# Kernel optimization log

Hardware: AMD Instinct MI355X
Metric: run time of the kernel (lower is better)

Reference implementation:

```python
import jax, jax.numpy as jnp
import numpy as np

N_NODES = 100000
N_EDGES = 1600000
C_IN, C_HID, C_OUT = 128, 64, 32


def setup_inputs() -> dict:
    key = jax.random.key(0)
    kx, ke, kw1, kw2 = jax.random.split(key, 4)
    x = jax.random.normal(kx, (N_NODES, C_IN), dtype=jnp.float32)
    edge_index = jax.random.randint(ke, (2, N_EDGES), 0, N_NODES, dtype=jnp.int64)
    # Glorot-ish init for the two GCNConv linear weights; PyG GCNConv bias inits to zero.
    W1 = jax.random.normal(kw1, (C_IN, C_HID), dtype=jnp.float32) / np.sqrt(C_IN)
    b1 = jnp.zeros((C_HID,), dtype=jnp.float32)
    W2 = jax.random.normal(kw2, (C_HID, C_OUT), dtype=jnp.float32) / np.sqrt(C_HID)
    b2 = jnp.zeros((C_OUT,), dtype=jnp.float32)
    return {"x": x, "edge_index": edge_index, "W1": W1, "b1": b1, "W2": W2, "b2": b2}


def _gcn_conv(x, W, b, src, dst, num_nodes):
    """PyG GCNConv: add self-loops, symmetric norm D^-1/2 A D^-1/2, linear, aggregate, bias."""
    xw = x @ W  # [N, out]
    # degree at destination, including the self-loop contribution of 1 per node
    deg = jnp.zeros((num_nodes,), xw.dtype).at[dst].add(1.0) + 1.0
    dinv = jax.lax.rsqrt(deg)  # deg >= 1 thanks to self-loops
    norm = dinv[src] * dinv[dst]  # [E]
    # scatter-add messages from source nodes into destination nodes
    out = jnp.zeros_like(xw).at[dst].add(norm[:, None] * xw[src])
    # self-loop term: norm_ii = dinv[i]^2
    out = out + (dinv * dinv)[:, None] * xw
    return out + b


def reference(x, edge_index, W1, b1, W2, b2):
    src, dst = edge_index[0], edge_index[1]
    h = _gcn_conv(x, W1, b1, src, dst, N_NODES)
    h = jax.nn.relu(h)
    # Dropout(0.1) is identity in eval mode (deterministic reference)
    out = _gcn_conv(h, W2, b2, src, dst, N_NODES)
    return out
```

## Files before the change

kernel.cpp:

```cpp
#include <hip/hip_runtime.h>
#include <hip/hip_bf16.h>


#define C_IN  128
#define C_HID 64
#define C_OUT 32
#define BK_SHIFT 10
#define BK_NODES (1 << BK_SHIFT)
#define BK_MAXB  128
#define EPB 2048

typedef unsigned short ushort_t;
typedef __attribute__((ext_vector_type(8))) short bf16x8;
typedef __attribute__((ext_vector_type(4))) float f32x4;

__device__ inline ushort_t f2bf(float f) {
    __hip_bfloat16 b = __float2bfloat16(f);
    return *reinterpret_cast<ushort_t*>(&b);
}
__device__ inline float bflo(unsigned int v) { return __uint_as_float(v << 16); }
__device__ inline float bfhi(unsigned int v) { return __uint_as_float(v & 0xffff0000u); }


__global__ __launch_bounds__(256) void bucket_edges(
        const int* __restrict__ src, const int* __restrict__ dst,
        int* __restrict__ bcur, unsigned int* __restrict__ bucketed,
        int cap, int E, int nb) {
    __shared__ unsigned int stage[EPB];
    __shared__ unsigned char bkt[EPB];
    __shared__ int cnt[BK_MAXB];
    __shared__ int lofs[BK_MAXB];
    __shared__ int base[BK_MAXB];
    int tid = threadIdx.x;
    for (int i = tid; i < nb; i += 256) cnt[i] = 0;
    __syncthreads();
    int e0 = blockIdx.x * EPB;
    int myb[8]; int myr[8]; unsigned int mys[8];
    #pragma unroll
    for (int i = 0; i < 8; ++i) {
        int e = e0 + i * 256 + tid;
        if (e < E) {
            int d = dst[e];
            int s = src[e];
            int b = d >> BK_SHIFT;
            myb[i] = b;
            mys[i] = (unsigned int)s | ((unsigned int)(d & (BK_NODES - 1)) << 17);
            myr[i] = atomicAdd(&cnt[b], 1);
        } else myb[i] = -1;
    }
    __syncthreads();
    if (tid < 64) {
        int b0 = 2 * tid, b1 = 2 * tid + 1;
        int c0 = (b0 < nb) ? cnt[b0] : 0;
        int c1 = (b1 < nb) ? cnt[b1] : 0;
        int p = c0 + c1;
        int s = p;
        #pragma unroll
        for (int off = 1; off < 64; off <<= 1) {
            int t = __shfl_up(s, off, 64);
            if (tid >= off) s += t;
        }
        if (b0 < nb) lofs[b0] = s - p;
        if (b1 < nb) lofs[b1] = s - c1;
    }
    __syncthreads();
    #pragma unroll
    for (int i = 0; i < 8; ++i) {
        if (myb[i] >= 0) {
            int p = lofs[myb[i]] + myr[i];
            stage[p] = mys[i];
            bkt[p] = (unsigned char)myb[i];
        }
    }
    for (int i = tid; i < nb; i += 256)
        base[i] = atomicAdd(&bcur[i], cnt[i]);
    __syncthreads();
    int total = min(EPB, E - e0);
    for (int p = tid; p < total; p += 256) {
        int b = bkt[p];
        int di = base[b] + (p - lofs[b]);
        if (di < cap)
            bucketed[(size_t)b * cap + di] = stage[p];
    }
}

__global__ void scan_eb(const int* __restrict__ bcur, int* __restrict__ ebase,
                        int* __restrict__ offsets, int cap, int nb, int n) {
    __shared__ int wsum[2];
    int tid = threadIdx.x;
    int lane = tid & 63, wid = tid >> 6;
    int v = (tid < nb) ? min(bcur[tid], cap) : 0;
    int s = v;
    #pragma unroll
    for (int off = 1; off < 64; off <<= 1) {
        int t = __shfl_up(s, off, 64);
        if (lane >= off) s += t;
    }
    if (lane == 63) wsum[wid] = s;
    __syncthreads();
    int incl = s + ((wid == 1) ? wsum[0] : 0);
    if (tid < nb) ebase[tid] = incl - v;
    if (tid == nb - 1) { ebase[nb] = incl; offsets[n] = incl; }
}

__global__ __launch_bounds__(1024) void fill_csr_fused(
        const unsigned int* __restrict__ bucketed, const int* __restrict__ ebase,
        int* __restrict__ offsets, float* __restrict__ dinv,
        int* __restrict__ csr_src, int cap, int n) {
    __shared__ int hist[BK_NODES];
    __shared__ int wsum[16];
    int tid = threadIdx.x, lane = tid & 63, wid = tid >> 6;
    int b = blockIdx.x;
    int node0 = b << BK_SHIFT;
    int nn = min(BK_NODES, n - node0);
    int eb = ebase[b];
    int cnt = ebase[b + 1] - eb;
    const unsigned int* bp = bucketed + (size_t)b * cap;
    hist[tid] = 0;
    __syncthreads();
    for (int e = tid; e < cnt; e += 1024)
        atomicAdd(&hist[bp[e] >> 17], 1);
    __syncthreads();
    int v = hist[tid];
    int s = v;
    #pragma unroll
    for (int off = 1; off < 64; off <<= 1) {
        int t = __shfl_up(s, off, 64);
        if (lane >= off) s += t;
    }
    if (lane == 63) wsum[wid] = s;
    __syncthreads();
    if (wid == 0 && lane < 16) {
        int ws = wsum[lane];
        #pragma unroll
        for (int off = 1; off < 16; off <<= 1) {
            int t = __shfl_up(ws, off, 64);
            if (lane >= off) ws += t;
        }
        wsum[lane] = ws;
    }
    __syncthreads();
    int wpre = (wid > 0) ? wsum[wid - 1] : 0;
    int excl = wpre + s - v;
    if (tid < nn) {
        offsets[node0 + tid] = eb + excl;
        dinv[node0 + tid] = rsqrtf((float)v + 1.0f);
    }
    __syncthreads();
    hist[tid] = eb + excl;
    __syncthreads();
    for (int e = tid; e < cnt; e += 1024) {
        unsigned int u = bp[e];
        int pos = atomicAdd(&hist[u >> 17], 1);
        csr_src[pos] = (int)(u & 0x1FFFFu);
    }
}

__global__ void count_deg(const int* __restrict__ dst, int* __restrict__ deg, int E) {
    int idx = blockIdx.x * blockDim.x + threadIdx.x;
    int stride = gridDim.x * blockDim.x;
    for (int e = idx; e < E; e += stride)
        atomicAdd(&deg[dst[e]], 1);
}

__global__ void fill_csr(const int* __restrict__ src, const int* __restrict__ dst,
                         int* __restrict__ cursor, int* __restrict__ csr_src, int E) {
    int idx = blockIdx.x * blockDim.x + threadIdx.x;
    int stride = gridDim.x * blockDim.x;
    for (int e = idx; e < E; e += stride) {
        int pos = atomicAdd(&cursor[dst[e]], 1);
        csr_src[pos] = src[e];
    }
}

__global__ void scan_blocks(const int* __restrict__ deg, int* __restrict__ offsets,
                            int* __restrict__ bsums, float* __restrict__ dinv, int n) {
    __shared__ int wsum[16];
    int tid = threadIdx.x, lane = tid & 63, wid = tid >> 6;
    int i = blockIdx.x * 1024 + tid;
    int v = (i < n) ? deg[i] : 0;
    if (i < n) dinv[i] = rsqrtf((float)v + 1.0f);
    int s = v;
    #pragma unroll
    for (int off = 1; off < 64; off <<= 1) {
        int t = __shfl_up(s, off, 64);
        if (lane >= off) s += t;
    }
    if (lane == 63) wsum[wid] = s;
    __syncthreads();
    if (wid == 0 && lane < 16) {
        int ws = wsum[lane];
        #pragma unroll
        for (int off = 1; off < 16; off <<= 1) {
            int t = __shfl_up(ws, off, 64);
            if (lane >= off) ws += t;
        }
        wsum[lane] = ws;
        if (lane == 15) bsums[blockIdx.x] = ws;
    }
    __syncthreads();
    int wpre = (wid > 0) ? wsum[wid - 1] : 0;
    if (i < n) offsets[i] = wpre + s - v;
}

__global__ void scan_bsums(int* __restrict__ bsums, int nb) {
    __shared__ int wsum[16];
    int tid = threadIdx.x, lane = tid & 63, wid = tid >> 6;
    int v = (tid < nb) ? bsums[tid] : 0;
    int s = v;
    #pragma unroll
    for (int off = 1; off < 64; off <<= 1) {
        int t = __shfl_up(s, off, 64);
        if (lane >= off) s += t;
    }
    if (lane == 63) wsum[wid] = s;
    __syncthreads();
    if (wid == 0 && lane < 16) {
        int ws = wsum[lane];
        #pragma unroll
        for (int off = 1; off < 16; off <<= 1) {
            int t = __shfl_up(ws, off, 64);
            if (lane >= off) ws += t;
        }
        wsum[lane] = ws;
    }
    __syncthreads();
    int wpre = (wid > 0) ? wsum[wid - 1] : 0;
    if (tid < nb) bsums[tid] = wpre + s - v;
}

__global__ void scan_add(int* __restrict__ offsets, const int* __restrict__ bsums,
                         int n, int E) {
    int i = blockIdx.x * 1024 + threadIdx.x;
    if (i < n) offsets[i] += bsums[blockIdx.x];
    if (i == 0) offsets[n] = E;
}

__global__ __launch_bounds__(256) void gemm1_mfma(
        const float* __restrict__ x, const float* __restrict__ W1,
        const float* __restrict__ dinv, ushort_t* __restrict__ xws_bf, int n) {
    __shared__ ushort_t Xs[64 * 136];
    __shared__ ushort_t Wl[16 * 64 * 8];
    int tid = threadIdx.x;
    {
        const float4* Wv = reinterpret_cast<const float4*>(W1);
        #pragma unroll
        for (int p = 0; p < 8; ++p) {
            int idx = p * 256 + tid;
            float4 w = Wv[idx];
            int k = idx >> 4;
            int c0 = (idx & 15) * 4;
            ushort_t* d = &Wl[(k >> 3) * 512 + c0 * 8 + (k & 7)];
            d[0]  = f2bf(w.x);
            d[8]  = f2bf(w.y);
            d[16] = f2bf(w.z);
            d[24] = f2bf(w.w);
        }
    }
    int row0 = blockIdx.x * 64;
    {
        const float4* xv = reinterpret_cast<const float4*>(x + (size_t)row0 * C_IN);
        int maxv = min(64, n - row0) * (C_IN / 4);
        #pragma unroll
        for (int p = 0; p < 8; ++p) {
            int idx = p * 256 + tid;
            float4 v = (idx < maxv) ? xv[idx] : float4{0.f, 0.f, 0.f, 0.f};
            int row = idx >> 5, k4 = idx & 31;
            ushort4 pk;
            pk.x = f2bf(v.x); pk.y = f2bf(v.y); pk.z = f2bf(v.z); pk.w = f2bf(v.w);
            *reinterpret_cast<ushort4*>(&Xs[row * 136 + k4 * 4]) = pk;
        }
    }
    __syncthreads();
    int wid = tid >> 6, lane = tid & 63;
    int rbase = wid * 16;
    int l15 = lane & 15, kgrp = lane >> 4;
    f32x4 acc0 = {0.f, 0.f, 0.f, 0.f}, acc1 = acc0, acc2 = acc0, acc3 = acc0;
    #pragma unroll
    for (int kc = 0; kc < 4; ++kc) {
        bf16x8 a = *reinterpret_cast<const bf16x8*>(&Xs[(rbase + l15) * 136 + kc * 32 + kgrp * 8]);
        const ushort_t* wb = &Wl[(kc * 4 + kgrp) * 512 + l15 * 8];
        bf16x8 b0 = *reinterpret_cast<const bf16x8*>(wb);
        bf16x8 b1 = *reinterpret_cast<const bf16x8*>(wb + 128);
        bf16x8 b2 = *reinterpret_cast<const bf16x8*>(wb + 256);
        bf16x8 b3 = *reinterpret_cast<const bf16x8*>(wb + 384);
        acc0 = __builtin_amdgcn_mfma_f32_16x16x32_bf16(a, b0, acc0, 0, 0, 0);
        acc1 = __builtin_amdgcn_mfma_f32_16x16x32_bf16(a, b1, acc1, 0, 0, 0);
        acc2 = __builtin_amdgcn_mfma_f32_16x16x32_bf16(a, b2, acc2, 0, 0, 0);
        acc3 = __builtin_amdgcn_mfma_f32_16x16x32_bf16(a, b3, acc3, 0, 0, 0);
    }
    #pragma unroll
    for (int j = 0; j < 4; ++j) {
        int row = row0 + rbase + kgrp * 4 + j;
        if (row < n) {
            float di = dinv[row];
            ushort_t* o = &xws_bf[(size_t)row * C_HID + l15];
            o[0]  = f2bf(di * acc0[j]);
            o[16] = f2bf(di * acc1[j]);
            o[32] = f2bf(di * acc2[j]);
            o[48] = f2bf(di * acc3[j]);
        }
    }
}


__global__ __launch_bounds__(256) void gemm2(
        const ushort_t* __restrict__ h_bf, const float* __restrict__ W2,
        const float* __restrict__ dinv, ushort_t* __restrict__ xws2_bf, int n) {
    __shared__ float Ws[C_HID * C_OUT];
    __shared__ float Hs[128 * C_HID];
    int tid = threadIdx.x;
    {
        const float4* Wv = reinterpret_cast<const float4*>(W2);
        float4* Wsv = reinterpret_cast<float4*>(Ws);
        #pragma unroll
        for (int p = 0; p < (C_HID * C_OUT / 4) / 256; ++p)
            Wsv[p * 256 + tid] = Wv[p * 256 + tid];
    }
    int row0 = blockIdx.x * 128;
    {
        const uint4* hv = reinterpret_cast<const uint4*>(h_bf + (size_t)row0 * C_HID);
        float4* Hsv = reinterpret_cast<float4*>(Hs);
        int maxe = min(128, n - row0) * (C_HID / 8);
        #pragma unroll
        for (int p = 0; p < 4; ++p) {
            int idx = p * 256 + tid;
            uint4 raw = (idx < maxe) ? hv[idx] : uint4{0u, 0u, 0u, 0u};
            float4 lo, hi;
            lo.x = bflo(raw.x); lo.y = bfhi(raw.x);
            lo.z = bflo(raw.y); lo.w = bfhi(raw.y);
            hi.x = bflo(raw.z); hi.y = bfhi(raw.z);
            hi.z = bflo(raw.w); hi.w = bfhi(raw.w);
            Hsv[idx * 2] = lo;
            Hsv[idx * 2 + 1] = hi;
        }
    }
    __syncthreads();
    int wid = tid >> 6, lane = tid & 63;
    int col = lane & 31, rh = lane >> 5;
    int rbase = wid * 32 + rh * 16;
    float acc[16];
    #pragma unroll
    for (int r = 0; r < 16; ++r) acc[r] = 0.f;
    const float4* Hsv = reinterpret_cast<const float4*>(Hs);
    #pragma unroll 2
    for (int k4 = 0; k4 < C_HID / 4; ++k4) {
        float w0 = Ws[(k4 * 4 + 0) * C_OUT + col];
        float w1 = Ws[(k4 * 4 + 1) * C_OUT + col];
        float w2 = Ws[(k4 * 4 + 2) * C_OUT + col];
        float w3 = Ws[(k4 * 4 + 3) * C_OUT + col];
        #pragma unroll
        for (int r = 0; r < 16; ++r) {
            float4 hv = Hsv[(rbase + r) * (C_HID / 4) + k4];
            acc[r] += hv.x * w0 + hv.y * w1 + hv.z * w2 + hv.w * w3;
        }
    }
    #pragma unroll
    for (int r = 0; r < 16; ++r) {
        int row = row0 + rbase + r;
        if (row < n) xws2_bf[(size_t)row * C_OUT + col] = f2bf(dinv[row] * acc[r]);
    }
}


__global__ void agg1(const ushort_t* __restrict__ xws_bf, const float* __restrict__ dinv,
                     const int* __restrict__ offsets, const int* __restrict__ csr_src,
                     const float* __restrict__ b1, ushort_t* __restrict__ h_bf, int n) {
    int wid = threadIdx.x >> 6, lane = threadIdx.x & 63;
    int half = lane >> 5, c2 = lane & 31;
    const unsigned int* xu = reinterpret_cast<const unsigned int*>(xws_bf);
    float2 bb = *reinterpret_cast<const float2*>(&b1[2 * c2]);
    for (int base = (blockIdx.x * 4 + wid) * 2; base < n; base += gridDim.x * 8) {
        int i = base + half;
        if (i < n) {
            int beg = offsets[i], end = offsets[i + 1];
            float di = dinv[i];
            unsigned int sv = xu[(size_t)i * 32 + c2];
            float a0 = bflo(sv), a1 = bfhi(sv);
            int k = beg;
            for (; k + 8 <= end; k += 8) {
                int s0 = csr_src[k + 0];
                int s1 = csr_src[k + 1];
                int s2 = csr_src[k + 2];
                int s3 = csr_src[k + 3];
                int s4 = csr_src[k + 4];
                int s5 = csr_src[k + 5];
                int s6 = csr_src[k + 6];
                int s7 = csr_src[k + 7];
                unsigned int v0 = xu[(size_t)s0 * 32 + c2];
                unsigned int v1 = xu[(size_t)s1 * 32 + c2];
                unsigned int v2 = xu[(size_t)s2 * 32 + c2];
                unsigned int v3 = xu[(size_t)s3 * 32 + c2];
                unsigned int v4 = xu[(size_t)s4 * 32 + c2];
                unsigned int v5 = xu[(size_t)s5 * 32 + c2];
                unsigned int v6 = xu[(size_t)s6 * 32 + c2];
                unsigned int v7 = xu[(size_t)s7 * 32 + c2];
                a0 += ((bflo(v0) + bflo(v1)) + (bflo(v2) + bflo(v3)))
                    + ((bflo(v4) + bflo(v5)) + (bflo(v6) + bflo(v7)));
                a1 += ((bfhi(v0) + bfhi(v1)) + (bfhi(v2) + bfhi(v3)))
                    + ((bfhi(v4) + bfhi(v5)) + (bfhi(v6) + bfhi(v7)));
            }
            for (; k + 4 <= end; k += 4) {
                int s0 = csr_src[k + 0];
                int s1 = csr_src[k + 1];
                int s2 = csr_src[k + 2];
                int s3 = csr_src[k + 3];
                unsigned int v0 = xu[(size_t)s0 * 32 + c2];
                unsigned int v1 = xu[(size_t)s1 * 32 + c2];
                unsigned int v2 = xu[(size_t)s2 * 32 + c2];
                unsigned int v3 = xu[(size_t)s3 * 32 + c2];
                a0 += (bflo(v0) + bflo(v1)) + (bflo(v2) + bflo(v3));
                a1 += (bfhi(v0) + bfhi(v1)) + (bfhi(v2) + bfhi(v3));
            }
            for (; k < end; ++k) {
                int s = csr_src[k];
                unsigned int v = xu[(size_t)s * 32 + c2];
                a0 += bflo(v); a1 += bfhi(v);
            }
            float r0 = fmaxf(di * a0 + bb.x, 0.f);
            float r1 = fmaxf(di * a1 + bb.y, 0.f);
            unsigned int pk = (unsigned int)f2bf(r0) | ((unsigned int)f2bf(r1) << 16);
            *reinterpret_cast<unsigned int*>(&h_bf[(size_t)i * C_HID + 2 * c2]) = pk;
        }
    }
}

__global__ void agg2(const ushort_t* __restrict__ xws2_bf, const float* __restrict__ dinv,
                     const int* __restrict__ offsets, const int* __restrict__ csr_src,
                     const float* __restrict__ b2, float* __restrict__ out, int n) {
    int wid = threadIdx.x >> 6, lane = threadIdx.x & 63;
    int q = lane >> 4, c2 = lane & 15;
    const unsigned int* xu = reinterpret_cast<const unsigned int*>(xws2_bf);
    float2 bb = *reinterpret_cast<const float2*>(&b2[2 * c2]);
    for (int base = (blockIdx.x * 4 + wid) * 4; base < n; base += gridDim.x * 16) {
        int i = base + q;
        if (i < n) {
            int beg = offsets[i], end = offsets[i + 1];
            float di = dinv[i];
            unsigned int sv = xu[(size_t)i * 16 + c2];
            float a0 = bflo(sv), a1 = bfhi(sv);
            int k = beg;
            for (; k + 8 <= end; k += 8) {
                int s0 = csr_src[k + 0];
                int s1 = csr_src[k + 1];
                int s2 = csr_src[k + 2];
                int s3 = csr_src[k + 3];
                int s4 = csr_src[k + 4];
                int s5 = csr_src[k + 5];
                int s6 = csr_src[k + 6];
                int s7 = csr_src[k + 7];
                unsigned int v0 = xu[(size_t)s0 * 16 + c2];
                unsigned int v1 = xu[(size_t)s1 * 16 + c2];
                unsigned int v2 = xu[(size_t)s2 * 16 + c2];
                unsigned int v3 = xu[(size_t)s3 * 16 + c2];
                unsigned int v4 = xu[(size_t)s4 * 16 + c2];
                unsigned int v5 = xu[(size_t)s5 * 16 + c2];
                unsigned int v6 = xu[(size_t)s6 * 16 + c2];
                unsigned int v7 = xu[(size_t)s7 * 16 + c2];
                a0 += ((bflo(v0) + bflo(v1)) + (bflo(v2) + bflo(v3)))
                    + ((bflo(v4) + bflo(v5)) + (bflo(v6) + bflo(v7)));
                a1 += ((bfhi(v0) + bfhi(v1)) + (bfhi(v2) + bfhi(v3)))
                    + ((bfhi(v4) + bfhi(v5)) + (bfhi(v6) + bfhi(v7)));
            }
            for (; k + 4 <= end; k += 4) {
                int s0 = csr_src[k + 0];
                int s1 = csr_src[k + 1];
                int s2 = csr_src[k + 2];
                int s3 = csr_src[k + 3];
                unsigned int v0 = xu[(size_t)s0 * 16 + c2];
                unsigned int v1 = xu[(size_t)s1 * 16 + c2];
                unsigned int v2 = xu[(size_t)s2 * 16 + c2];
                unsigned int v3 = xu[(size_t)s3 * 16 + c2];
                a0 += (bflo(v0) + bflo(v1)) + (bflo(v2) + bflo(v3));
                a1 += (bfhi(v0) + bfhi(v1)) + (bfhi(v2) + bfhi(v3));
            }
            for (; k < end; ++k) {
                int s = csr_src[k];
                unsigned int v = xu[(size_t)s * 16 + c2];
                a0 += bflo(v); a1 += bfhi(v);
            }
            float2 r;
            r.x = di * a0 + bb.x;
            r.y = di * a1 + bb.y;
            *reinterpret_cast<float2*>(&out[(size_t)i * C_OUT + 2 * c2]) = r;
        }
    }
}

extern "C" void kernel_launch(void* const* d_in, const int* in_sizes, int n_in,
                              void* d_out, int out_size, void* d_ws, size_t ws_size,
                              hipStream_t stream) {
    const float* x  = (const float*)d_in[0];
    const int*   ei = (const int*)d_in[1];
    const float* W1 = (const float*)d_in[2];
    const float* b1 = (const float*)d_in[3];
    const float* W2 = (const float*)d_in[4];
    const float* b2 = (const float*)d_in[5];
    float* out = (float*)d_out;

    const int N = in_sizes[0] / C_IN;
    const int E = in_sizes[1] / 2;
    const int* src = ei;
    const int* dst = ei + E;

    const int NB = (N + BK_NODES - 1) >> BK_SHIFT;
    const int CAP = (2 * (E / NB) + 1023) & ~1023;

    char* ws = (char*)d_ws;
    size_t off = 0;
    auto alloc = [&](size_t bytes) { char* p = ws + off; off += (bytes + 255) & ~(size_t)255; return p; };
    ushort_t* xw_bf  = (ushort_t*)alloc((size_t)N * C_HID * 2);
    ushort_t* h_bf   = (ushort_t*)alloc((size_t)N * C_HID * 2);
    int*   deg     = (int*)alloc((size_t)N * 4);
    float* dinv    = (float*)alloc((size_t)N * 4);
    int*   offsets = (int*)alloc((size_t)(N + 1) * 4);
    int*   cursor  = (int*)alloc((size_t)N * 4);
    int*   csr_src = (int*)alloc((size_t)E * 4);
    int*   bsums   = (int*)alloc(4096);
    int*   bcur    = (int*)alloc((size_t)BK_MAXB * 4);
    int*   ebase   = (int*)alloc((size_t)(BK_MAXB + 1) * 4);
    unsigned int* bucketed = (unsigned int*)alloc((size_t)NB * CAP * 4);
    bool use_bucket = (off <= ws_size) && (NB <= BK_MAXB) && (N < (1 << 17));

    const int nb1024 = (N + 1023) / 1024;

    if (use_bucket) {
        hipMemsetAsync(bcur, 0, (size_t)NB * 4, stream);
        bucket_edges<<<(E + EPB - 1) / EPB, 256, 0, stream>>>(
            src, dst, bcur, bucketed, CAP, E, NB);
        scan_eb<<<1, 128, 0, stream>>>(bcur, ebase, offsets, CAP, NB, N);
        fill_csr_fused<<<NB, 1024, 0, stream>>>(bucketed, ebase, offsets, dinv,
                                                csr_src, CAP, N);
    } else {
        hipMemsetAsync(deg, 0, (size_t)N * 4, stream);
        count_deg<<<2048, 256, 0, stream>>>(dst, deg, E);
        scan_blocks<<<nb1024, 1024, 0, stream>>>(deg, offsets, bsums, dinv, N);
        scan_bsums<<<1, 1024, 0, stream>>>(bsums, nb1024);
        scan_add<<<nb1024, 1024, 0, stream>>>(offsets, bsums, N, E);
        hipMemcpyAsync(cursor, offsets, (size_t)N * 4, hipMemcpyDeviceToDevice, stream);
        fill_csr<<<2048, 256, 0, stream>>>(src, dst, cursor, csr_src, E);
    }

    gemm1_mfma<<<(N + 63) / 64, 256, 0, stream>>>(x, W1, dinv, xw_bf, N);
    agg1<<<2048, 256, 0, stream>>>(xw_bf, dinv, offsets, csr_src, b1, h_bf, N);
    gemm2<<<(N + 127) / 128, 256, 0, stream>>>(h_bf, W2, dinv, xw_bf, N);
    agg2<<<2048, 256, 0, stream>>>(xw_bf, dinv, offsets, csr_src, b2, out, N);
}
```

Measured before the change: 149.0 us.

## Use MFMA for second GEMM and fold bucket scan into CSR fill

The second linear layer now runs on bf16 MFMA instructions instead of scalar fp32 FMAs, with tiles of 64 rows. The weights are repacked into an MFMA-friendly shared layout, and the activations are staged directly as bf16 without unpacking to float. The separate bucket-offset scan kernel is removed: each fill_csr_fused block redoes the small 128-entry scan itself. The memset is replaced by a tiny zeroing kernel. Together these cut launch count and ALU time in gemm2, at the cost of redundant per-block scans and bf16 rounding of W2.

```diff
diff --git a/kernel.cpp b/kernel.cpp
--- a/kernel.cpp
+++ b/kernel.cpp
@@ -21,6 +21,11 @@
 __device__ inline float bflo(unsigned int v) { return __uint_as_float(v << 16); }
 __device__ inline float bfhi(unsigned int v) { return __uint_as_float(v & 0xffff0000u); }
 
+
+__global__ void zero_bcur(int* __restrict__ bcur, int nb) {
+    int i = threadIdx.x;
+    if (i < nb) bcur[i] = 0;
+}
 
 __global__ __launch_bounds__(256) void bucket_edges(
         const int* __restrict__ src, const int* __restrict__ dst,
@@ -84,40 +89,41 @@
     }
 }
 
-__global__ void scan_eb(const int* __restrict__ bcur, int* __restrict__ ebase,
-                        int* __restrict__ offsets, int cap, int nb, int n) {
-    __shared__ int wsum[2];
-    int tid = threadIdx.x;
-    int lane = tid & 63, wid = tid >> 6;
-    int v = (tid < nb) ? min(bcur[tid], cap) : 0;
-    int s = v;
-    #pragma unroll
-    for (int off = 1; off < 64; off <<= 1) {
-        int t = __shfl_up(s, off, 64);
-        if (lane >= off) s += t;
-    }
-    if (lane == 63) wsum[wid] = s;
-    __syncthreads();
-    int incl = s + ((wid == 1) ? wsum[0] : 0);
-    if (tid < nb) ebase[tid] = incl - v;
-    if (tid == nb - 1) { ebase[nb] = incl; offsets[n] = incl; }
-}
-
 __global__ __launch_bounds__(1024) void fill_csr_fused(
-        const unsigned int* __restrict__ bucketed, const int* __restrict__ ebase,
+        const unsigned int* __restrict__ bucketed, const int* __restrict__ bcur,
         int* __restrict__ offsets, float* __restrict__ dinv,
-        int* __restrict__ csr_src, int cap, int n) {
+        int* __restrict__ csr_src, int cap, int nb, int n) {
     __shared__ int hist[BK_NODES];
     __shared__ int wsum[16];
+    __shared__ int sEb[BK_MAXB + 1];
+    __shared__ int sW[2];
     int tid = threadIdx.x, lane = tid & 63, wid = tid >> 6;
     int b = blockIdx.x;
+    int v128 = 0, s128 = 0;
+    if (tid < 128) {
+        v128 = (tid < nb) ? min(bcur[tid], cap) : 0;
+        s128 = v128;
+        #pragma unroll
+        for (int off = 1; off < 64; off <<= 1) {
+            int t = __shfl_up(s128, off, 64);
+            if (lane >= off) s128 += t;
+        }
+        if (lane == 63) sW[wid] = s128;
+    }
+    __syncthreads();
+    if (tid < 128) {
+        int incl = s128 + ((wid == 1) ? sW[0] : 0);
+        sEb[tid] = incl - v128;
+        if (tid == nb - 1) sEb[nb] = incl;
+    }
+    hist[tid] = 0;
+    __syncthreads();
+    int eb = sEb[b];
+    int cnt = sEb[b + 1] - eb;
+    if (b == 0 && tid == 0) offsets[n] = sEb[nb];
     int node0 = b << BK_SHIFT;
     int nn = min(BK_NODES, n - node0);
-    int eb = ebase[b];
-    int cnt = ebase[b + 1] - eb;
     const unsigned int* bp = bucketed + (size_t)b * cap;
-    hist[tid] = 0;
-    __syncthreads();
     for (int e = tid; e < cnt; e += 1024)
         atomicAdd(&hist[bp[e] >> 17], 1);
     __syncthreads();
@@ -303,62 +309,62 @@
     }
 }
 
-
-__global__ __launch_bounds__(256) void gemm2(
+__global__ __launch_bounds__(256) void gemm2_mfma(
         const ushort_t* __restrict__ h_bf, const float* __restrict__ W2,
         const float* __restrict__ dinv, ushort_t* __restrict__ xws2_bf, int n) {
-    __shared__ float Ws[C_HID * C_OUT];
-    __shared__ float Hs[128 * C_HID];
+    __shared__ ushort_t Hs[64 * 72];
+    __shared__ ushort_t Wl[8 * 32 * 8];
     int tid = threadIdx.x;
     {
         const float4* Wv = reinterpret_cast<const float4*>(W2);
-        float4* Wsv = reinterpret_cast<float4*>(Ws);
-        #pragma unroll
-        for (int p = 0; p < (C_HID * C_OUT / 4) / 256; ++p)
-            Wsv[p * 256 + tid] = Wv[p * 256 + tid];
-    }
-    int row0 = blockIdx.x * 128;
+        #pragma unroll
+        for (int p = 0; p < 2; ++p) {
+            int idx = p * 256 + tid;
+            float4 w = Wv[idx];
+            int k = idx >> 3;
+            int c0 = (idx & 7) * 4;
+            ushort_t* d = &Wl[(k >> 3) * 256 + c0 * 8 + (k & 7)];
+            d[0]  = f2bf(w.x);
+            d[8]  = f2bf(w.y);
+            d[16] = f2bf(w.z);
+            d[24] = f2bf(w.w);
+        }
+    }
+    int row0 = blockIdx.x * 64;
     {
         const uint4* hv = reinterpret_cast<const uint4*>(h_bf + (size_t)row0 * C_HID);
-        float4* Hsv = reinterpret_cast<float4*>(Hs);
-        int maxe = min(128, n - row0) * (C_HID / 8);
-        #pragma unroll
-        for (int p = 0; p < 4; ++p) {
+        int maxv = min(64, n - row0) * 8;
+        #pragma unroll
+        for (int p = 0; p < 2; ++p) {
             int idx = p * 256 + tid;
-            uint4 raw = (idx < maxe) ? hv[idx] : uint4{0u, 0u, 0u, 0u};
-            float4 lo, hi;
-            lo.x = bflo(raw.x); lo.y = bfhi(raw.x);
-            lo.z = bflo(raw.y); lo.w = bfhi(raw.y);
-            hi.x = bflo(raw.z); hi.y = bfhi(raw.z);
-            hi.z = bflo(raw.w); hi.w = bfhi(raw.w);
-            Hsv[idx * 2] = lo;
-            Hsv[idx * 2 + 1] = hi;
+            uint4 v = (idx < maxv) ? hv[idx] : uint4{0u, 0u, 0u, 0u};
+            int row = idx >> 3, c16 = idx & 7;
+            *reinterpret_cast<uint4*>(&Hs[row * 72 + c16 * 8]) = v;
         }
     }
     __syncthreads();
     int wid = tid >> 6, lane = tid & 63;
-    int col = lane & 31, rh = lane >> 5;
-    int rbase = wid * 32 + rh * 16;
-    float acc[16];
-    #pragma unroll
-    for (int r = 0; r < 16; ++r) acc[r] = 0.f;
-    const float4* Hsv = reinterpret_cast<const float4*>(Hs);
-    #pragma unroll 2
-    for (int k4 = 0; k4 < C_HID / 4; ++k4) {
-        float w0 = Ws[(k4 * 4 + 0) * C_OUT + col];
-        float w1 = Ws[(k4 * 4 + 1) * C_OUT + col];
-        float w2 = Ws[(k4 * 4 + 2) * C_OUT + col];
-        float w3 = Ws[(k4 * 4 + 3) * C_OUT + col];
-        #pragma unroll
-        for (int r = 0; r < 16; ++r) {
-            float4 hv = Hsv[(rbase + r) * (C_HID / 4) + k4];
-            acc[r] += hv.x * w0 + hv.y * w1 + hv.z * w2 + hv.w * w3;
-        }
-    }
-    #pragma unroll
-    for (int r = 0; r < 16; ++r) {
-        int row = row0 + rbase + r;
-        if (row < n) xws2_bf[(size_t)row * C_OUT + col] = f2bf(dinv[row] * acc[r]);
+    int rbase = wid * 16;
+    int l15 = lane & 15, kgrp = lane >> 4;
+    f32x4 acc0 = {0.f, 0.f, 0.f, 0.f}, acc1 = acc0;
+    #pragma unroll
+    for (int kc = 0; kc < 2; ++kc) {
+        bf16x8 a = *reinterpret_cast<const bf16x8*>(&Hs[(rbase + l15) * 72 + kc * 32 + kgrp * 8]);
+        const ushort_t* wb = &Wl[(kc * 4 + kgrp) * 256 + l15 * 8];
+        bf16x8 b0 = *reinterpret_cast<const bf16x8*>(wb);
+        bf16x8 b1 = *reinterpret_cast<const bf16x8*>(wb + 128);
+        acc0 = __builtin_amdgcn_mfma_f32_16x16x32_bf16(a, b0, acc0, 0, 0, 0);
+        acc1 = __builtin_amdgcn_mfma_f32_16x16x32_bf16(a, b1, acc1, 0, 0, 0);
+    }
+    #pragma unroll
+    for (int j = 0; j < 4; ++j) {
+        int row = row0 + rbase + kgrp * 4 + j;
+        if (row < n) {
+            float di = dinv[row];
+            ushort_t* o = &xws2_bf[(size_t)row * C_OUT + l15];
+            o[0]  = f2bf(di * acc0[j]);
+            o[16] = f2bf(di * acc1[j]);
+        }
     }
 }
 
@@ -518,19 +524,17 @@
     int*   csr_src = (int*)alloc((size_t)E * 4);
     int*   bsums   = (int*)alloc(4096);
     int*   bcur    = (int*)alloc((size_t)BK_MAXB * 4);
-    int*   ebase   = (int*)alloc((size_t)(BK_MAXB + 1) * 4);
     unsigned int* bucketed = (unsigned int*)alloc((size_t)NB * CAP * 4);
     bool use_bucket = (off <= ws_size) && (NB <= BK_MAXB) && (N < (1 << 17));
 
     const int nb1024 = (N + 1023) / 1024;
 
     if (use_bucket) {
-        hipMemsetAsync(bcur, 0, (size_t)NB * 4, stream);
+        zero_bcur<<<1, 128, 0, stream>>>(bcur, NB);
         bucket_edges<<<(E + EPB - 1) / EPB, 256, 0, stream>>>(
             src, dst, bcur, bucketed, CAP, E, NB);
-        scan_eb<<<1, 128, 0, stream>>>(bcur, ebase, offsets, CAP, NB, N);
-        fill_csr_fused<<<NB, 1024, 0, stream>>>(bucketed, ebase, offsets, dinv,
-                                                csr_src, CAP, N);
+        fill_csr_fused<<<NB, 1024, 0, stream>>>(bucketed, bcur, offsets, dinv,
+                                                csr_src, CAP, NB, N);
     } else {
         hipMemsetAsync(deg, 0, (size_t)N * 4, stream);
         count_deg<<<2048, 256, 0, stream>>>(dst, deg, E);
@@ -543,6 +547,6 @@
 
     gemm1_mfma<<<(N + 63) / 64, 256, 0, stream>>>(x, W1, dinv, xw_bf, N);
     agg1<<<2048, 256, 0, stream>>>(xw_bf, dinv, offsets, csr_src, b1, h_bf, N);
-    gemm2<<<(N + 127) / 128, 256, 0, stream>>>(h_bf, W2, dinv, xw_bf, N);
+    gemm2_mfma<<<(N + 63) / 64, 256, 0, stream>>>(h_bf, W2, dinv, xw_bf, N);
     agg2<<<2048, 256, 0, stream>>>(xw_bf, dinv, offsets, csr_src, b2, out, N);
 }
```

After: 132.6 us. 1.12x faster.
